# Kernel tuning notes

Measured on AMD Instinct MI355X. Metric: run time of the kernel, lower is better.

## Reference

```python
import jax, jax.numpy as jnp
import numpy as np

HEADS = 16
DIM_HEAD = 64


def setup_inputs() -> dict:
    key = jax.random.key(0)
    k1, k2, k3, k4 = jax.random.split(key, 4)
    b, sq, skv, dim = 2, 2048, 2048, 1024
    inner = HEADS * DIM_HEAD
    return {
        "x_q": jax.random.normal(k1, (b, sq, dim), dtype=jnp.float32),
        "x_kv": jax.random.normal(k2, (b, skv, dim), dtype=jnp.float32),
        "W_qkv": jax.random.normal(k3, (dim, 3 * inner), dtype=jnp.float32) * (dim ** -0.5),
        "W_out": jax.random.normal(k4, (inner, dim), dtype=jnp.float32) * (inner ** -0.5),
        "b_out": jnp.zeros((dim,), dtype=jnp.float32),
    }


def reference(x_q, x_kv, W_qkv, W_out, b_out):
    b, sq, dim = x_q.shape
    skv = x_kv.shape[1]
    inner = HEADS * DIM_HEAD
    scale = DIM_HEAD ** -0.5
    # to_qkv on concat([x_q, x_kv], seq) as in the original (bias-free linear)
    qkv = jnp.concatenate([x_q, x_kv], axis=1) @ W_qkv  # [b, sq+skv, 3*inner]
    q, k, v = jnp.split(qkv, 3, axis=-1)
    q = q[:, :sq].reshape(b, sq, HEADS, DIM_HEAD).transpose(0, 2, 1, 3)   # [b,h,sq,d]
    k = k[:, sq:].reshape(b, skv, HEADS, DIM_HEAD).transpose(0, 2, 1, 3)  # [b,h,skv,d]
    v = v[:, sq:].reshape(b, skv, HEADS, DIM_HEAD).transpose(0, 2, 1, 3)  # [b,h,skv,d]
    dots = jnp.einsum('bhqd,bhkd->bhqk', q, k) * scale
    attn = jax.nn.softmax(dots, axis=-1)  # dropout p=0.0 -> identity
    out = jnp.einsum('bhqk,bhkd->bhqd', attn, v)
    out = out.transpose(0, 2, 1, 3).reshape(b, sq, inner)
    return out @ W_out + b_out
```

## Files before the change

kernel.cpp:

```cpp
#include <hip/hip_runtime.h>


typedef __attribute__((ext_vector_type(8))) short short8;
typedef __attribute__((ext_vector_type(4))) short short4v;
typedef __attribute__((ext_vector_type(4))) float floatx4;
typedef __attribute__((ext_vector_type(16))) float floatx16;

#define QSCALE 0.18033688f

#if __has_builtin(__builtin_amdgcn_exp2f)
#define EXP2(x) __builtin_amdgcn_exp2f(x)
#else
#define EXP2(x) exp2f(x)
#endif

__device__ __forceinline__ ushort f2b(float f) {
  union { float f; unsigned u; } x; x.f = f;
  unsigned r = (x.u + 0x7fffu + ((x.u >> 16) & 1u)) >> 16;
  return (ushort)r;
}

__device__ __forceinline__ unsigned f2b2(float a, float b) {
  union { float f; unsigned u; } x, y; x.f = a; y.f = b;
  return __builtin_amdgcn_perm(y.u + 0x8000u, x.u + 0x8000u, 0x07060302u);
}

__device__ __forceinline__ unsigned cvtpk(float a, float b) {
  unsigned r;
  asm("v_cvt_pk_bf16_f32 %0, %1, %2" : "=v"(r) : "v"(a), "v"(b));
  return r;
}

#define GLL(gp, lp)                                                            \
  __builtin_amdgcn_global_load_lds(                                            \
      (const __attribute__((address_space(1))) void*)(gp),                     \
      (__attribute__((address_space(3))) void*)(lp), 16, 0, 0)

__global__ void prep(const float* __restrict__ xq, const float* __restrict__ xkv,
                     ushort* __restrict__ oq, ushort* __restrict__ okv,
                     const float* __restrict__ Wqkv, ushort* __restrict__ WqkvT,
                     const float* __restrict__ Wout, ushort* __restrict__ WoutT) {
  __shared__ float tile[32][33];
  int bid = blockIdx.x;
  const int n = 4096 * 1024;
  if (bid < 2048) {
    bool lo = bid < 1024;
    const float* in = lo ? xq : xkv;
    ushort* out = lo ? oq : okv;
    int b2 = lo ? bid : bid - 1024;
    int stride = 1024 * 256 * 4;
    for (int i = (b2 * 256 + (int)threadIdx.x) * 4; i < n; i += stride) {
      float4 v = *(const float4*)(in + i);
      uint2 o;
      o.x = f2b2(v.x, v.y);
      o.y = f2b2(v.z, v.w);
      *(uint2*)(out + i) = o;
    }
    return;
  }
  int tb = bid - 2048;
  int bx = tb & 127, by = tb >> 7;
  bool first = bx < 96;
  const float* in = first ? Wqkv : Wout;
  ushort* out = first ? WqkvT : WoutT;
  int N = first ? 3072 : 1024;
  int bxx = first ? bx : bx - 96;
  int k0 = by * 32, n0 = bxx * 32;
  int tx = threadIdx.x & 31, ty = threadIdx.x >> 5;
#pragma unroll
  for (int i = 0; i < 32; i += 8)
    tile[ty + i][tx] = in[(size_t)(k0 + ty + i) * N + n0 + tx];
  __syncthreads();
#pragma unroll
  for (int i = 0; i < 32; i += 8)
    out[(size_t)(n0 + ty + i) * 1024 + k0 + tx] = f2b(tile[tx][ty + i]);
}

__global__ __launch_bounds__(256, 3) void gemm_qkv(
    const ushort* __restrict__ Aq, const ushort* __restrict__ Akv,
    const ushort* __restrict__ Bt,
    ushort* __restrict__ Cq, ushort* __restrict__ Ck, ushort* __restrict__ Cv) {
  __shared__ __align__(16) ushort smem[17408];
  ushort* Asb = smem;
  ushort* Bsb = smem + 8192;
  const int n0 = blockIdx.x * 128, m0 = blockIdx.y * 128;
  const ushort* A = (blockIdx.x >= 8) ? Akv : Aq;
  const int t = threadIdx.x;
  const int w = t >> 6, lane = t & 63, dl = lane & 15, g = lane >> 4;
  const int wm = (w >> 1) * 64, wn = (w & 1) * 64;
  const int K = 1024;

  auto stage = [&](int buf, int k0) {
#pragma unroll
    for (int p = 0; p < 2; p++) {
      int j = t + p * 256;
      int row = j >> 2, slot = j & 3, c = (slot - row) & 3;
      GLL(A + (size_t)(m0 + row) * K + k0 + c * 8, &Asb[buf * 4096 + j * 8]);
    }
#pragma unroll
    for (int p = 0; p < 2; p++) {
      int j = t + p * 256;
      int row = j >> 2, slot = j & 3, c = (slot - row) & 3;
      GLL(Bt + (size_t)(n0 + row) * K + k0 + c * 8, &Bsb[buf * 4096 + j * 8]);
    }
  };

  const floatx4 fz = {0.f, 0.f, 0.f, 0.f};
  floatx4 acc[4][4];
#pragma unroll
  for (int i = 0; i < 4; i++)
#pragma unroll
    for (int j = 0; j < 4; j++) acc[i][j] = fz;

  stage(0, 0);
  for (int kt = 0; kt < 32; kt++) {
    int cur = kt & 1;
    __builtin_amdgcn_s_waitcnt(0);
    __syncthreads();
    if (kt + 1 < 32) stage(cur ^ 1, (kt + 1) * 32);
    short8 af[4], bf[4];
#pragma unroll
    for (int mt = 0; mt < 4; mt++) {
      int row = wm + mt * 16 + dl;
      af[mt] = *(const short8*)&Asb[cur * 4096 + row * 32 + ((g + row) & 3) * 8];
    }
#pragma unroll
    for (int nt = 0; nt < 4; nt++) {
      int row = wn + nt * 16 + dl;
      bf[nt] = *(const short8*)&Bsb[cur * 4096 + row * 32 + ((g + row) & 3) * 8];
    }
#pragma unroll
    for (int mt = 0; mt < 4; mt++)
#pragma unroll
      for (int nt = 0; nt < 4; nt++)
        acc[mt][nt] = __builtin_amdgcn_mfma_f32_16x16x32_bf16(af[mt], bf[nt], acc[mt][nt], 0, 0, 0);
  }

  if (blockIdx.x < 16) {
#pragma unroll
    for (int mt = 0; mt < 4; mt++)
#pragma unroll
      for (int nt = 0; nt < 4; nt++) {
        int gcol = n0 + wn + nt * 16 + dl;
        int row0 = m0 + wm + mt * 16 + g * 4;
        if (gcol < 1024) {
#pragma unroll
          for (int r = 0; r < 4; r++)
            Cq[(size_t)(row0 + r) * 1024 + gcol] = f2b(acc[mt][nt][r] * QSCALE);
        } else {
#pragma unroll
          for (int r = 0; r < 4; r++)
            Ck[(size_t)(row0 + r) * 1024 + gcol - 1024] = f2b(acc[mt][nt][r]);
        }
      }
  } else {
    __syncthreads();
#pragma unroll
    for (int mt = 0; mt < 4; mt++)
#pragma unroll
      for (int nt = 0; nt < 4; nt++) {
        int ncol = wn + nt * 16 + dl;
        int mrow = wm + mt * 16 + g * 4;
        uint2 pk;
        pk.x = f2b2(acc[mt][nt][0], acc[mt][nt][1]);
        pk.y = f2b2(acc[mt][nt][2], acc[mt][nt][3]);
        *(uint2*)&smem[ncol * 136 + mrow] = pk;
      }
    __syncthreads();
    int hd0 = n0 - 2048;
    int bb = m0 >> 11;
    int kv0 = m0 & 2047;
#pragma unroll
    for (int p = 0; p < 8; p++) {
      int j = t + p * 256;
      int row = j >> 4, c = j & 15;
      short8 v = *(const short8*)&smem[row * 136 + c * 8];
      *(short8*)(Cv + ((size_t)(bb * 1024 + hd0 + row)) * 2048 + kv0 + c * 8) = v;
    }
  }
}

__global__ __launch_bounds__(256, 3) void gemm_out(
    const ushort* __restrict__ A, const ushort* __restrict__ Bt,
    float* __restrict__ C, const float* __restrict__ bias) {
  __shared__ __align__(16) ushort As[2][128 * 64];
  __shared__ __align__(16) ushort Bs[2][64 * 64];
  const int n0 = blockIdx.x * 64, m0 = blockIdx.y * 128;
  const int t = threadIdx.x;
  const int w = t >> 6, lane = t & 63, dl = lane & 15, g = lane >> 4;
  const int wm = (w >> 1) * 64, wn = (w & 1) * 32;
  const int K = 1024;

  auto stage = [&](int buf, int k0) {
#pragma unroll
    for (int p = 0; p < 4; p++) {
      int j = t + p * 256;
      int row = j >> 3, slot = j & 7, c = (slot - row) & 7;
      GLL(A + (size_t)(m0 + row) * K + k0 + c * 8, &As[buf][j * 8]);
    }
#pragma unroll
    for (int p = 0; p < 2; p++) {
      int j = t + p * 256;
      int row = j >> 3, slot = j & 7, c = (slot - row) & 7;
      GLL(Bt + (size_t)(n0 + row) * K + k0 + c * 8, &Bs[buf][j * 8]);
    }
  };

  const floatx4 fz = {0.f, 0.f, 0.f, 0.f};
  floatx4 acc[4][2];
#pragma unroll
  for (int i = 0; i < 4; i++)
#pragma unroll
    for (int j = 0; j < 2; j++) acc[i][j] = fz;

  stage(0, 0);
  for (int kt = 0; kt < 16; kt++) {
    int cur = kt & 1;
    __builtin_amdgcn_s_waitcnt(0);
    __syncthreads();
    if (kt + 1 < 16) stage(cur ^ 1, (kt + 1) * 64);
#pragma unroll
    for (int ks = 0; ks < 2; ks++) {
      short8 af[4], bf[2];
#pragma unroll
      for (int mt = 0; mt < 4; mt++) {
        int row = wm + mt * 16 + dl;
        af[mt] = *(const short8*)&As[cur][row * 64 + ((ks * 4 + g + row) & 7) * 8];
      }
#pragma unroll
      for (int nt = 0; nt < 2; nt++) {
        int row = wn + nt * 16 + dl;
        bf[nt] = *(const short8*)&Bs[cur][row * 64 + ((ks * 4 + g + row) & 7) * 8];
      }
#pragma unroll
      for (int mt = 0; mt < 4; mt++)
#pragma unroll
        for (int nt = 0; nt < 2; nt++)
          acc[mt][nt] = __builtin_amdgcn_mfma_f32_16x16x32_bf16(af[mt], bf[nt], acc[mt][nt], 0, 0, 0);
    }
  }
#pragma unroll
  for (int mt = 0; mt < 4; mt++)
#pragma unroll
    for (int nt = 0; nt < 2; nt++) {
      int gcol = n0 + wn + nt * 16 + dl;
      int row0 = m0 + wm + mt * 16 + g * 4;
      float badd = bias[gcol];
#pragma unroll
      for (int r = 0; r < 4; r++)
        C[(size_t)(row0 + r) * 1024 + gcol] = acc[mt][nt][r] + badd;
    }
}

__global__ __launch_bounds__(256, 2) void attn(
    const ushort* __restrict__ Qb,
    const ushort* __restrict__ Kb,
    const ushort* __restrict__ Vt,
    ushort* __restrict__ Ob) {
  __shared__ __align__(16) ushort Ks[2][64 * 64];
  __shared__ __align__(16) ushort Vs[2][64 * 64];

  const int bh = blockIdx.x, b = bh >> 4, h = bh & 15;
  const int q0 = blockIdx.y * 128;
  const int t = threadIdx.x, w = t >> 6, lane = t & 63;
  const int l31 = lane & 31, l5 = lane >> 5;

  const ushort* Kg = Kb + (size_t)(b * 2048) * 1024 + h * 64;
  const ushort* Vg = Vt + (size_t)(b * 1024 + h * 64) * 2048;

  short8 bq[4];
  {
    int qa = q0 + w * 32 + l31;
    const ushort* qrow = Qb + (size_t)(b * 2048 + qa) * 1024 + h * 64;
#pragma unroll
    for (int ks = 0; ks < 4; ks++)
      bq[ks] = *(const short8*)(qrow + ks * 16 + l5 * 8);
  }

  auto stageK = [&](int buf, int kv0) {
#pragma unroll
    for (int p = 0; p < 2; p++) {
      int j = t + p * 256;
      int row = j >> 3, slot = j & 7, c = (slot - row) & 7;
      GLL(Kg + (size_t)(kv0 + row) * 1024 + c * 8, &Ks[buf][j * 8]);
    }
  };
  auto stageV = [&](int buf, int kv0) {
#pragma unroll
    for (int p = 0; p < 2; p++) {
      int j = t + p * 256;
      int row = j >> 3, slot = j & 7, c = (slot - row) & 7;
      GLL(Vg + (size_t)row * 2048 + kv0 + c * 8, &Vs[buf][j * 8]);
    }
  };
  stageK(0, 0);
  stageV(0, 0);

  floatx16 o2[2];
#pragma unroll
  for (int m2 = 0; m2 < 2; m2++)
#pragma unroll
    for (int r = 0; r < 16; r++) o2[m2][r] = 0.f;
  floatx4 l4 = {0.f, 0.f, 0.f, 0.f};

  for (int it = 0; it < 32; it++) {
    int cur = it & 1;
    __builtin_amdgcn_s_waitcnt(0);
    __syncthreads();
    if (it + 1 < 32) { stageK(cur ^ 1, (it + 1) * 64); stageV(cur ^ 1, (it + 1) * 64); }

    floatx16 s2[2];
#pragma unroll
    for (int m2 = 0; m2 < 2; m2++)
#pragma unroll
      for (int r = 0; r < 16; r++) s2[m2][r] = 0.f;
#pragma unroll
    for (int ks = 0; ks < 4; ks++)
#pragma unroll
      for (int m2 = 0; m2 < 2; m2++) {
        int row = m2 * 32 + l31;
        short8 a = *(const short8*)&Ks[cur][row * 64 + ((ks * 2 + l5 + row) & 7) * 8];
        s2[m2] = __builtin_amdgcn_mfma_f32_32x32x16_bf16(a, bq[ks], s2[m2], 0, 0, 0);
      }

#pragma unroll
    for (int m2 = 0; m2 < 2; m2++)
#pragma unroll
      for (int r = 0; r < 16; r++) s2[m2][r] = EXP2(s2[m2][r]);
#pragma unroll
    for (int r = 0; r < 16; r++) l4[r & 3] += s2[0][r] + s2[1][r];

    short8 bp[4];
#pragma unroll
    for (int m2 = 0; m2 < 2; m2++) {
      unsigned pk[8];
#pragma unroll
      for (int p = 0; p < 8; p++)
        pk[p] = cvtpk(s2[m2][2 * p], s2[m2][2 * p + 1]);
#pragma unroll
      for (int hf = 0; hf < 2; hf++) {
        unsigned x0 = pk[hf * 4 + 0], y0 = pk[hf * 4 + 2];
        unsigned x1 = pk[hf * 4 + 1], y1 = pk[hf * 4 + 3];
        asm("v_permlane32_swap_b32 %0, %1" : "+v"(x0), "+v"(y0));
        asm("v_permlane32_swap_b32 %0, %1" : "+v"(x1), "+v"(y1));
        union { unsigned u[4]; short8 s8; } fu;
        fu.u[0] = x0; fu.u[1] = x1; fu.u[2] = y0; fu.u[3] = y1;
        bp[m2 * 2 + hf] = fu.s8;
      }
    }

#pragma unroll
    for (int kt = 0; kt < 4; kt++)
#pragma unroll
      for (int m2 = 0; m2 < 2; m2++) {
        int row = m2 * 32 + l31;
        short8 av = *(const short8*)&Vs[cur][row * 64 + ((kt * 2 + l5 + row) & 7) * 8];
        o2[m2] = __builtin_amdgcn_mfma_f32_32x32x16_bf16(av, bp[kt], o2[m2], 0, 0, 0);
      }
  }

  float l = (l4[0] + l4[1]) + (l4[2] + l4[3]);
  l += __shfl_xor(l, 32);
  float inv_l = 1.f / l;

  __syncthreads();
  ushort* Ot = &Ks[0][0];
  {
    int q = w * 32 + l31;
#pragma unroll
    for (int m2 = 0; m2 < 2; m2++)
#pragma unroll
      for (int pp = 0; pp < 4; pp++) {
        uint2 pk2;
        pk2.x = cvtpk(o2[m2][4 * pp + 0] * inv_l, o2[m2][4 * pp + 1] * inv_l);
        pk2.y = cvtpk(o2[m2][4 * pp + 2] * inv_l, o2[m2][4 * pp + 3] * inv_l);
        int s = m2 * 8 + 2 * pp + l5;
        *(uint2*)&Ot[q * 64 + ((s + q) & 15) * 4] = pk2;
      }
  }
  asm volatile("" ::: "memory");
#pragma unroll
  for (int p = 0; p < 4; p++) {
    int j = lane + p * 64;
    int r32 = j >> 3, c = j & 7;
    int qr = w * 32 + r32;
    short4v lo = *(const short4v*)&Ot[qr * 64 + ((2 * c + qr) & 15) * 4];
    short4v hi = *(const short4v*)&Ot[qr * 64 + ((2 * c + 1 + qr) & 15) * 4];
    short8 v = {lo.x, lo.y, lo.z, lo.w, hi.x, hi.y, hi.z, hi.w};
    *(short8*)(Ob + (size_t)(b * 2048 + q0 + qr) * 1024 + h * 64 + c * 8) = v;
  }
}

extern "C" void kernel_launch(void* const* d_in, const int* in_sizes, int n_in,
                              void* d_out, int out_size, void* d_ws, size_t ws_size,
                              hipStream_t stream) {
  const float* x_q  = (const float*)d_in[0];
  const float* x_kv = (const float*)d_in[1];
  const float* Wqkv = (const float*)d_in[2];
  const float* Wout = (const float*)d_in[3];
  const float* bout = (const float*)d_in[4];
  float* out = (float*)d_out;

  char* p = (char*)d_ws;
  ushort* Xq    = (ushort*)p; p += (size_t)4096 * 1024 * 2;
  ushort* Xkv   = (ushort*)p; p += (size_t)4096 * 1024 * 2;
  ushort* WqkvT = (ushort*)p; p += (size_t)3072 * 1024 * 2;
  ushort* WoutT = (ushort*)p; p += (size_t)1024 * 1024 * 2;
  ushort* Qb    = (ushort*)p; p += (size_t)4096 * 1024 * 2;
  ushort* Kb    = (ushort*)p; p += (size_t)4096 * 1024 * 2;
  ushort* Vt    = (ushort*)p; p += (size_t)2 * 1024 * 2048 * 2;
  ushort* Ob    = (ushort*)p; p += (size_t)4096 * 1024 * 2;

  prep<<<6144, 256, 0, stream>>>(x_q, x_kv, Xq, Xkv, Wqkv, WqkvT, Wout, WoutT);
  gemm_qkv<<<dim3(24, 32), 256, 0, stream>>>(Xq, Xkv, WqkvT, Qb, Kb, Vt);
  attn<<<dim3(32, 16), 256, 0, stream>>>(Qb, Kb, Vt, Ob);
  gemm_out<<<dim3(16, 32), 256, 0, stream>>>(Ob, WoutT, out, bout);
}
```

Baseline: 191.8 us.

## Double KV tile to 128 per iteration with interleaved QK/softmax and setprio

Raises the attention KV tile from 64 to 128 rows, halving the number of loop iterations and barriers. Shared memory for K/V double buffers doubles, and the swizzle now adds row>>3 to spread bank accesses. The QK^T, exp and pack steps are processed one 32-row sub-tile at a time to limit live registers, and s_setprio brackets the MFMA sections to favour matrix issue across waves. The costs are higher LDS use, which may cut occupancy below the two-blocks-per-CU target, and more live bp registers.

```diff
diff --git a/kernel.cpp b/kernel.cpp
--- a/kernel.cpp
+++ b/kernel.cpp
@@ -257,8 +257,8 @@
     const ushort* __restrict__ Kb,
     const ushort* __restrict__ Vt,
     ushort* __restrict__ Ob) {
-  __shared__ __align__(16) ushort Ks[2][64 * 64];
-  __shared__ __align__(16) ushort Vs[2][64 * 64];
+  __shared__ __align__(16) ushort Ks[2][128 * 64];
+  __shared__ __align__(16) ushort Vs[2][64 * 128];
 
   const int bh = blockIdx.x, b = bh >> 4, h = bh & 15;
   const int q0 = blockIdx.y * 128;
@@ -279,17 +279,17 @@
 
   auto stageK = [&](int buf, int kv0) {
 #pragma unroll
-    for (int p = 0; p < 2; p++) {
-      int j = t + p * 256;
-      int row = j >> 3, slot = j & 7, c = (slot - row) & 7;
+    for (int p = 0; p < 4; p++) {
+      int j = t + p * 256;
+      int row = j >> 3, slot = j & 7, c = (slot - row - (row >> 3)) & 7;
       GLL(Kg + (size_t)(kv0 + row) * 1024 + c * 8, &Ks[buf][j * 8]);
     }
   };
   auto stageV = [&](int buf, int kv0) {
 #pragma unroll
-    for (int p = 0; p < 2; p++) {
-      int j = t + p * 256;
-      int row = j >> 3, slot = j & 7, c = (slot - row) & 7;
+    for (int p = 0; p < 4; p++) {
+      int j = t + p * 256;
+      int row = j >> 4, slot = j & 15, c = (slot - row - (row >> 3)) & 15;
       GLL(Vg + (size_t)row * 2048 + kv0 + c * 8, &Vs[buf][j * 8]);
     }
   };
@@ -303,40 +303,35 @@
     for (int r = 0; r < 16; r++) o2[m2][r] = 0.f;
   floatx4 l4 = {0.f, 0.f, 0.f, 0.f};
 
-  for (int it = 0; it < 32; it++) {
+  for (int it = 0; it < 16; it++) {
     int cur = it & 1;
     __builtin_amdgcn_s_waitcnt(0);
     __syncthreads();
-    if (it + 1 < 32) { stageK(cur ^ 1, (it + 1) * 64); stageV(cur ^ 1, (it + 1) * 64); }
-
-    floatx16 s2[2];
-#pragma unroll
-    for (int m2 = 0; m2 < 2; m2++)
-#pragma unroll
-      for (int r = 0; r < 16; r++) s2[m2][r] = 0.f;
-#pragma unroll
-    for (int ks = 0; ks < 4; ks++)
-#pragma unroll
-      for (int m2 = 0; m2 < 2; m2++) {
-        int row = m2 * 32 + l31;
-        short8 a = *(const short8*)&Ks[cur][row * 64 + ((ks * 2 + l5 + row) & 7) * 8];
-        s2[m2] = __builtin_amdgcn_mfma_f32_32x32x16_bf16(a, bq[ks], s2[m2], 0, 0, 0);
-      }
-
-#pragma unroll
-    for (int m2 = 0; m2 < 2; m2++)
-#pragma unroll
-      for (int r = 0; r < 16; r++) s2[m2][r] = EXP2(s2[m2][r]);
-#pragma unroll
-    for (int r = 0; r < 16; r++) l4[r & 3] += s2[0][r] + s2[1][r];
-
-    short8 bp[4];
-#pragma unroll
-    for (int m2 = 0; m2 < 2; m2++) {
+    if (it + 1 < 16) { stageK(cur ^ 1, (it + 1) * 128); stageV(cur ^ 1, (it + 1) * 128); }
+
+    short8 bp[8];
+#pragma unroll
+    for (int m2 = 0; m2 < 4; m2++) {
+      floatx16 s;
+#pragma unroll
+      for (int r = 0; r < 16; r++) s[r] = 0.f;
+      int row = m2 * 32 + l31;
+      __builtin_amdgcn_s_setprio(1);
+#pragma unroll
+      for (int ks = 0; ks < 4; ks++) {
+        short8 a = *(const short8*)
+            &Ks[cur][row * 64 + ((ks * 2 + l5 + row + (row >> 3)) & 7) * 8];
+        s = __builtin_amdgcn_mfma_f32_32x32x16_bf16(a, bq[ks], s, 0, 0, 0);
+      }
+      __builtin_amdgcn_s_setprio(0);
+#pragma unroll
+      for (int r = 0; r < 16; r++) s[r] = EXP2(s[r]);
+#pragma unroll
+      for (int r = 0; r < 16; r++) l4[r & 3] += s[r];
       unsigned pk[8];
 #pragma unroll
       for (int p = 0; p < 8; p++)
-        pk[p] = cvtpk(s2[m2][2 * p], s2[m2][2 * p + 1]);
+        pk[p] = cvtpk(s[2 * p], s[2 * p + 1]);
 #pragma unroll
       for (int hf = 0; hf < 2; hf++) {
         unsigned x0 = pk[hf * 4 + 0], y0 = pk[hf * 4 + 2];
@@ -349,14 +344,17 @@
       }
     }
 
-#pragma unroll
-    for (int kt = 0; kt < 4; kt++)
+    __builtin_amdgcn_s_setprio(1);
+#pragma unroll
+    for (int kt = 0; kt < 8; kt++)
 #pragma unroll
       for (int m2 = 0; m2 < 2; m2++) {
         int row = m2 * 32 + l31;
-        short8 av = *(const short8*)&Vs[cur][row * 64 + ((kt * 2 + l5 + row) & 7) * 8];
+        short8 av = *(const short8*)
+            &Vs[cur][row * 128 + ((kt * 2 + l5 + row + (row >> 3)) & 15) * 8];
         o2[m2] = __builtin_amdgcn_mfma_f32_32x32x16_bf16(av, bp[kt], o2[m2], 0, 0, 0);
       }
+    __builtin_amdgcn_s_setprio(0);
   }
 
   float l = (l4[0] + l4[1]) + (l4[2] + l4[3]);
```

Result: no change. 189.5 us (-1.2%).
